# Performance work log

Hardware: AMD Instinct MI355X
Metric: run time of the kernel (lower is better)

Reference implementation:

```python
import jax, jax.numpy as jnp
import numpy as np

B, T = 256, 511          # batch, seq_len (512 - 1)
V = 128                  # tune_vocab_size
RV, MV, KV = 30, 20, 40  # rhythm/meter/key vocab sizes
E, ET = 16, 32           # context emb dim, tune emb dim
D = 3 * E + ET           # 80, LSTM input dim
H = 256                  # LSTM hidden


def setup_inputs() -> dict:
    key = jax.random.key(0)
    ks = jax.random.split(key, 14)
    s = 0.05
    return {
        "tune": jax.random.randint(ks[0], (B, T), 0, V + 1, dtype=jnp.int32),
        "rhythm": jax.random.randint(ks[1], (B, 1), 0, RV + 1, dtype=jnp.int32),
        "meter": jax.random.randint(ks[2], (B, 1), 0, MV + 1, dtype=jnp.int32),
        "key": jax.random.randint(ks[3], (B, 1), 0, KV + 1, dtype=jnp.int32),
        "tune_length": jax.random.randint(ks[4], (B, 1), 1, T, dtype=jnp.int32),
        # learned parameters
        "emb_rhythm": jax.random.normal(ks[5], (RV + 1, E), jnp.float32) * s,
        "emb_meter": jax.random.normal(ks[6], (MV + 1, E), jnp.float32) * s,
        "emb_key": jax.random.normal(ks[7], (KV + 1, E), jnp.float32) * s,
        "emb_tune": jax.random.normal(ks[8], (V + 1, ET), jnp.float32) * s,
        "W": jax.random.normal(ks[9], (D, 4 * H), jnp.float32) * s,   # input kernel (gates i,f,c,o)
        "U": jax.random.normal(ks[10], (H, 4 * H), jnp.float32) * s,  # recurrent kernel
        "b": jax.random.normal(ks[11], (4 * H,), jnp.float32) * s,
        "Wd": jax.random.normal(ks[12], (H, V), jnp.float32) * s,     # output dense
        "bd": jax.random.normal(ks[13], (V,), jnp.float32) * s,
    }


def reference(tune, rhythm, meter, key, tune_length,
              emb_rhythm, emb_meter, emb_key, emb_tune, W, U, b, Wd, bd):
    Bc, Tc = tune.shape
    Hc = U.shape[0]
    # conditioning context, repeated over time: [B, 48]
    ctx = jnp.concatenate(
        [emb_rhythm[rhythm[:, 0]], emb_meter[meter[:, 0]], emb_key[key[:, 0]]], axis=-1)
    # full LSTM input: [B, T, 80]
    x = jnp.concatenate(
        [jnp.broadcast_to(ctx[:, None, :], (Bc, Tc, ctx.shape[-1])), emb_tune[tune]], axis=-1)
    # sequence mask: step t valid iff t < tune_length  -> [B, T]
    mask = jnp.arange(Tc, dtype=tune_length.dtype)[None, :] < tune_length

    xs = jnp.swapaxes(x, 0, 1)   # [T, B, 80]
    ms = mask.T                  # [T, B]

    def step(carry, inp):
        h, c = carry
        xt, mt = inp
        z = xt @ W + h @ U + b                      # [B, 4H]
        i, f, g, o = jnp.split(z, 4, axis=-1)       # keras gate order i,f,c,o
        i = jax.nn.sigmoid(i)
        f = jax.nn.sigmoid(f)
        g = jnp.tanh(g)
        o = jax.nn.sigmoid(o)
        c_new = f * c + i * g
        h_new = o * jnp.tanh(c_new)
        m = mt[:, None]
        # masked steps: carry state through unchanged, output zeros
        h2 = jnp.where(m, h_new, h)
        c2 = jnp.where(m, c_new, c)
        out = jnp.where(m, h_new, jnp.zeros_like(h_new))
        return (h2, c2), out

    init = (jnp.zeros((Bc, Hc), x.dtype), jnp.zeros((Bc, Hc), x.dtype))
    _, ys = jax.lax.scan(step, init, (xs, ms))  # ys: [T, B, H]
    ys = jnp.swapaxes(ys, 0, 1)                 # [B, T, H]
    return ys @ Wd + bd                         # logits [B, T, V]
```

## Files before the change

### kernel.cpp

```cpp
#include <hip/hip_runtime.h>
#include <hip/hip_fp16.h>
#include <stdint.h>

#define BB 256
#define TT 511
#define VV 128
#define HH 256
#define G4 1024

typedef _Float16 h2_t __attribute__((ext_vector_type(2)));

__device__ __forceinline__ float fdot2(uint32_t a, uint32_t b, float c) {
  return __builtin_amdgcn_fdot2(__builtin_bit_cast(h2_t, a),
                                __builtin_bit_cast(h2_t, b), c, false);
}

__device__ __forceinline__ uint32_t pack2(float a, float b) {
  __half ha = __float2half(a), hb = __float2half(b);
  return (uint32_t)__half_as_ushort(ha) | ((uint32_t)__half_as_ushort(hb) << 16);
}


__global__ __launch_bounds__(1024) void prep_ctx_k(
    const int* __restrict__ rhythm, const int* __restrict__ meter, const int* __restrict__ keyi,
    const float* __restrict__ er, const float* __restrict__ em, const float* __restrict__ ek,
    const float* __restrict__ W, const float* __restrict__ bias, float* __restrict__ ctxW) {
  int b = blockIdx.x, j = threadIdx.x;
  int r = rhythm[b], m = meter[b], k = keyi[b];
  float acc = bias[j];
#pragma unroll
  for (int e = 0; e < 16; e++) acc += er[r*16+e] * W[(0+e)*G4 + j];
#pragma unroll
  for (int e = 0; e < 16; e++) acc += em[m*16+e] * W[(16+e)*G4 + j];
#pragma unroll
  for (int e = 0; e < 16; e++) acc += ek[k*16+e] * W[(32+e)*G4 + j];
  ctxW[b*G4 + j] = acc;
}

__global__ __launch_bounds__(1024) void prep_tune_k(
    const float* __restrict__ et, const float* __restrict__ W, float* __restrict__ tuneW) {
  int v = blockIdx.x, j = threadIdx.x;
  float acc = 0.f;
#pragma unroll
  for (int e = 0; e < 32; e++) acc += et[v*32+e] * W[(48+e)*G4 + j];
  tuneW[v*G4 + j] = acc;
}

__global__ __launch_bounds__(1024) void prep_U_k(
    const float* __restrict__ U, uint32_t* __restrict__ Up) {
  int kk = blockIdx.x, j = threadIdx.x;
  Up[kk*G4 + j] = pack2(U[(2*kk)*G4 + j], U[(2*kk+1)*G4 + j]);
}

__global__ __launch_bounds__(128) void prep_Wd_k(
    const float* __restrict__ Wd, uint32_t* __restrict__ Wdp) {
  int kp = blockIdx.x, v = threadIdx.x;
  Wdp[kp*VV + v] = pack2(Wd[(2*kp)*VV + v], Wd[(2*kp+1)*VV + v]);
}


#define NT 512
#define KREG 96
#define KLDS 32
#define RS 36
#define SMEM_BYTES (1024*RS*4 + 4096 + 512 + 2048)

__global__ __launch_bounds__(NT) void lstm_rec_k(
    const int* __restrict__ tune, const int* __restrict__ tlen,
    const uint32_t* __restrict__ Up, const float* __restrict__ ctxW,
    const float* __restrict__ tuneW, __half* __restrict__ h_hist) {
  extern __shared__ uint32_t smem[];
  uint32_t* Ulds = smem;
  float*    zbuf = (float*)(smem + 1024*RS);
  uint32_t* hpk  = (uint32_t*)(smem + 1024*RS + 1024);
  int*      tlds = (int*)(smem + 1024*RS + 1024 + 128);

  int b   = blockIdx.x;
  int tid = threadIdx.x;
  int L   = tlen[b];

  for (int i = tid; i < TT; i += NT) tlds[i] = tune[b*TT + i];
  if (tid < 128) hpk[tid] = 0u;

  uint32_t u0[KREG], u1[KREG];
#pragma unroll
  for (int kk = 0; kk < KREG; kk++) {
    u0[kk] = Up[kk*G4 + tid];
    u1[kk] = Up[kk*G4 + tid + NT];
  }
  for (int idx = tid; idx < KLDS*G4; idx += NT) {
    int kk = idx >> 10, j = idx & 1023;
    Ulds[j*RS + kk] = Up[(KREG+kk)*G4 + j];
  }
  float zc0 = ctxW[b*G4 + tid];
  float zc1 = ctxW[b*G4 + tid + NT];
  float cc  = 0.f;
  __syncthreads();

  const uint32_t* ur0 = Ulds + (size_t)tid*RS;
  const uint32_t* ur1 = Ulds + (size_t)(tid+NT)*RS;
  __half* hh_base = h_hist + (size_t)b*TT*HH;

  for (int t = 0; t < L; t++) {
    int v = tlds[t];
    float tw0 = tuneW[v*G4 + tid];
    float tw1 = tuneW[v*G4 + tid + NT];
    float a0 = 0.f, a1 = 0.f, d0 = 0.f, d1 = 0.f;
#pragma unroll
    for (int g = 0; g < KREG/4; g++) {
      uint4 h4 = *(const uint4*)(hpk + g*4);
      a0 = fdot2(h4.x, u0[4*g+0], a0);  a1 = fdot2(h4.x, u1[4*g+0], a1);
      d0 = fdot2(h4.y, u0[4*g+1], d0);  d1 = fdot2(h4.y, u1[4*g+1], d1);
      a0 = fdot2(h4.z, u0[4*g+2], a0);  a1 = fdot2(h4.z, u1[4*g+2], a1);
      d0 = fdot2(h4.w, u0[4*g+3], d0);  d1 = fdot2(h4.w, u1[4*g+3], d1);
    }
#pragma unroll
    for (int g = 0; g < KLDS/4; g++) {
      uint4 h4 = *(const uint4*)(hpk + KREG + g*4);
      uint4 ua = *(const uint4*)(ur0 + g*4);
      uint4 ub = *(const uint4*)(ur1 + g*4);
      a0 = fdot2(h4.x, ua.x, a0);  a1 = fdot2(h4.x, ub.x, a1);
      d0 = fdot2(h4.y, ua.y, d0);  d1 = fdot2(h4.y, ub.y, d1);
      a0 = fdot2(h4.z, ua.z, a0);  a1 = fdot2(h4.z, ub.z, a1);
      d0 = fdot2(h4.w, ua.w, d0);  d1 = fdot2(h4.w, ub.w, d1);
    }
    zbuf[tid]      = zc0 + tw0 + a0 + d0;
    zbuf[tid + NT] = zc1 + tw1 + a1 + d1;
    __syncthreads();
    if (tid < HH) {
      float zi = zbuf[tid];
      float zf = zbuf[tid + 256];
      float zg = zbuf[tid + 512];
      float zo = zbuf[tid + 768];
      float gi = 1.f / (1.f + __expf(-zi));
      float gf = 1.f / (1.f + __expf(-zf));
      float e2 = __expf(2.f*zg);
      float gg = (e2 - 1.f) / (e2 + 1.f);
      float go = 1.f / (1.f + __expf(-zo));
      cc = gf*cc + gi*gg;
      float ec = __expf(2.f*cc);
      float th = (ec - 1.f) / (ec + 1.f);
      float hv = go * th;
      __half hhv = __float2half(hv);
      ((__half*)hpk)[tid] = hhv;
      hh_base[(size_t)t*HH + tid] = hhv;
    }
    __syncthreads();
  }
}


__global__ __launch_bounds__(256) void out_gemm_k(
    const uint32_t* __restrict__ hsrc, const uint32_t* __restrict__ Wdp,
    const float* __restrict__ bd, const int* __restrict__ tlen,
    float* __restrict__ out) {
  __shared__ uint32_t A[64][128];
  int bb = blockIdx.x;
  int b  = bb >> 3, t0 = (bb & 7) << 6;
  int tid = threadIdx.x;
  int L = tlen[b];
  for (int idx = tid; idx < 64*128; idx += 256) {
    int r = idx >> 7, kp = idx & 127;
    int t = t0 + r;
    A[r][kp] = (t < TT) ? hsrc[((size_t)b*TT + t)*128 + kp] : 0u;
  }
  __syncthreads();
  int v = tid & 127, rg = tid >> 7;
  float acc[32];
#pragma unroll
  for (int r = 0; r < 32; r++) acc[r] = 0.f;
  for (int kb = 0; kb < 4; kb++) {
    uint32_t w[32];
#pragma unroll
    for (int q = 0; q < 32; q++) w[q] = Wdp[(kb*32+q)*VV + v];
#pragma unroll
    for (int r = 0; r < 32; r++) {
      const uint32_t* ar = &A[rg*32 + r][kb*32];
#pragma unroll
      for (int q4 = 0; q4 < 8; q4++) {
        uint4 a4 = *(const uint4*)(ar + q4*4);
        acc[r] = fdot2(a4.x, w[4*q4+0], acc[r]);
        acc[r] = fdot2(a4.y, w[4*q4+1], acc[r]);
        acc[r] = fdot2(a4.z, w[4*q4+2], acc[r]);
        acc[r] = fdot2(a4.w, w[4*q4+3], acc[r]);
      }
    }
  }
  float bias = bd[v];
#pragma unroll
  for (int r = 0; r < 32; r++) {
    int t = t0 + rg*32 + r;
    if (t < TT) {
      out[((size_t)b*TT + t)*VV + v] = (t < L) ? (acc[r] + bias) : bias;
    }
  }
}


extern "C" void kernel_launch(void* const* d_in, const int* in_sizes, int n_in,
                              void* d_out, int out_size, void* d_ws, size_t ws_size,
                              hipStream_t stream) {
  const int*   tune   = (const int*)d_in[0];
  const int*   rhythm = (const int*)d_in[1];
  const int*   meter  = (const int*)d_in[2];
  const int*   keyi   = (const int*)d_in[3];
  const int*   tlen   = (const int*)d_in[4];
  const float* er     = (const float*)d_in[5];
  const float* em     = (const float*)d_in[6];
  const float* ek     = (const float*)d_in[7];
  const float* et     = (const float*)d_in[8];
  const float* W      = (const float*)d_in[9];
  const float* U      = (const float*)d_in[10];
  const float* bias   = (const float*)d_in[11];
  const float* Wd     = (const float*)d_in[12];
  const float* bd     = (const float*)d_in[13];
  (void)in_sizes; (void)n_in; (void)out_size; (void)ws_size;

  char* ws = (char*)d_ws;
  uint32_t* Up    = (uint32_t*)(ws);
  float*    ctxW  = (float*)(ws + (512<<10));
  float*    tuneW = (float*)(ws + (512<<10) + (1024<<10));
  uint32_t* Wdp   = (uint32_t*)(ws + (512<<10) + (1024<<10) + (516<<10));

  hipFuncSetAttribute((const void*)lstm_rec_k,
                      hipFuncAttributeMaxDynamicSharedMemorySize, SMEM_BYTES);

  prep_ctx_k <<<BB,    1024, 0, stream>>>(rhythm, meter, keyi, er, em, ek, W, bias, ctxW);
  prep_tune_k<<<VV+1,  1024, 0, stream>>>(et, W, tuneW);
  prep_U_k   <<<128,   1024, 0, stream>>>(U, Up);
  prep_Wd_k  <<<128,   VV,   0, stream>>>(Wd, Wdp);
  lstm_rec_k <<<BB, NT, SMEM_BYTES, stream>>>(tune, tlen, Up, ctxW, tuneW, (__half*)d_out);
  out_gemm_k <<<BB*8,  256,  0, stream>>>((const uint32_t*)d_out, Wdp, bd, tlen, (float*)d_out);
}
```

Measured before the change: 951.6 us.

## Split recurrent matvec over K halves with readlane-broadcast hidden state

Restructures the LSTM recurrent matvec so each 256-thread half handles half of the hidden dimension and each thread computes four adjacent gate columns using uint4 register-resident weights. Hidden-state values are broadcast via readlane instead of repeated LDS vector loads, and partial sums from both halves are combined in the gate phase together with context terms now staged in LDS. This aims to reduce per-step LDS bandwidth, but raises register pressure and adds a cross-half reduction.

```diff
diff --git a/kernel.cpp b/kernel.cpp
--- a/kernel.cpp
+++ b/kernel.cpp
@@ -60,78 +60,88 @@
 
 
 #define NT 512
-#define KREG 96
-#define KLDS 32
-#define RS 36
-#define SMEM_BYTES (1024*RS*4 + 4096 + 512 + 2048)
+#define KREG 54
+#define KLDS 10
+#define ULDS_ROWS (2*KLDS)
+#define OFF_ZPART (ULDS_ROWS*G4)
+#define OFF_CTX   (OFF_ZPART + 2*G4)
+#define OFF_HBUF  (OFF_CTX + G4)
+#define OFF_TLDS  (OFF_HBUF + 128)
+#define SMEM_U32  (OFF_TLDS + 512)
+#define SMEM_BYTES (SMEM_U32*4)
 
 __global__ __launch_bounds__(NT) void lstm_rec_k(
     const int* __restrict__ tune, const int* __restrict__ tlen,
     const uint32_t* __restrict__ Up, const float* __restrict__ ctxW,
     const float* __restrict__ tuneW, __half* __restrict__ h_hist) {
   extern __shared__ uint32_t smem[];
-  uint32_t* Ulds = smem;
-  float*    zbuf = (float*)(smem + 1024*RS);
-  uint32_t* hpk  = (uint32_t*)(smem + 1024*RS + 1024);
-  int*      tlds = (int*)(smem + 1024*RS + 1024 + 128);
-
-  int b   = blockIdx.x;
-  int tid = threadIdx.x;
-  int L   = tlen[b];
+  uint32_t* Ulds   = smem;
+  float*    zpart  = (float*)(smem + OFF_ZPART);
+  float*    ctxlds = (float*)(smem + OFF_CTX);
+  uint32_t* hbuf   = smem + OFF_HBUF;
+  int*      tlds   = (int*)(smem + OFF_TLDS);
+
+  int b    = blockIdx.x;
+  int tid  = threadIdx.x;
+  int g    = tid >> 8;
+  int q    = tid & 255;
+  int lane = tid & 63;
+  int L    = tlen[b];
 
   for (int i = tid; i < TT; i += NT) tlds[i] = tune[b*TT + i];
-  if (tid < 128) hpk[tid] = 0u;
-
-  uint32_t u0[KREG], u1[KREG];
-#pragma unroll
-  for (int kk = 0; kk < KREG; kk++) {
-    u0[kk] = Up[kk*G4 + tid];
-    u1[kk] = Up[kk*G4 + tid + NT];
-  }
-  for (int idx = tid; idx < KLDS*G4; idx += NT) {
-    int kk = idx >> 10, j = idx & 1023;
-    Ulds[j*RS + kk] = Up[(KREG+kk)*G4 + j];
-  }
-  float zc0 = ctxW[b*G4 + tid];
-  float zc1 = ctxW[b*G4 + tid + NT];
-  float cc  = 0.f;
+  for (int i = tid; i < G4; i += NT) ctxlds[i] = ctxW[b*G4 + i];
+  if (tid < 128) hbuf[tid] = 0u;
+  for (int idx = tid; idx < ULDS_ROWS*G4; idx += NT) {
+    int row = idx >> 10, j = idx & 1023;
+    int gg = row / KLDS, r = row % KLDS;
+    Ulds[idx] = Up[(gg*64 + KREG + r)*G4 + j];
+  }
+
+  uint4 ureg[KREG];
+  {
+    const uint32_t* ubase = Up + (size_t)(g*64)*G4 + 4*q;
+#pragma unroll
+    for (int kk = 0; kk < KREG; kk++) ureg[kk] = *(const uint4*)(ubase + (size_t)kk*G4);
+  }
+  float cc = 0.f;
   __syncthreads();
 
-  const uint32_t* ur0 = Ulds + (size_t)tid*RS;
-  const uint32_t* ur1 = Ulds + (size_t)(tid+NT)*RS;
+  const uint32_t* uldsrow = Ulds + (size_t)(g*KLDS)*G4 + 4*q;
   __half* hh_base = h_hist + (size_t)b*TT*HH;
 
   for (int t = 0; t < L; t++) {
+    uint32_t vh = hbuf[g*64 + lane];
     int v = tlds[t];
-    float tw0 = tuneW[v*G4 + tid];
-    float tw1 = tuneW[v*G4 + tid + NT];
-    float a0 = 0.f, a1 = 0.f, d0 = 0.f, d1 = 0.f;
-#pragma unroll
-    for (int g = 0; g < KREG/4; g++) {
-      uint4 h4 = *(const uint4*)(hpk + g*4);
-      a0 = fdot2(h4.x, u0[4*g+0], a0);  a1 = fdot2(h4.x, u1[4*g+0], a1);
-      d0 = fdot2(h4.y, u0[4*g+1], d0);  d1 = fdot2(h4.y, u1[4*g+1], d1);
-      a0 = fdot2(h4.z, u0[4*g+2], a0);  a1 = fdot2(h4.z, u1[4*g+2], a1);
-      d0 = fdot2(h4.w, u0[4*g+3], d0);  d1 = fdot2(h4.w, u1[4*g+3], d1);
-    }
-#pragma unroll
-    for (int g = 0; g < KLDS/4; g++) {
-      uint4 h4 = *(const uint4*)(hpk + KREG + g*4);
-      uint4 ua = *(const uint4*)(ur0 + g*4);
-      uint4 ub = *(const uint4*)(ur1 + g*4);
-      a0 = fdot2(h4.x, ua.x, a0);  a1 = fdot2(h4.x, ub.x, a1);
-      d0 = fdot2(h4.y, ua.y, d0);  d1 = fdot2(h4.y, ub.y, d1);
-      a0 = fdot2(h4.z, ua.z, a0);  a1 = fdot2(h4.z, ub.z, a1);
-      d0 = fdot2(h4.w, ua.w, d0);  d1 = fdot2(h4.w, ub.w, d1);
-    }
-    zbuf[tid]      = zc0 + tw0 + a0 + d0;
-    zbuf[tid + NT] = zc1 + tw1 + a1 + d1;
+    float tw0, tw1, tw2, tw3;
+    if (tid < HH) {
+      const float* twp = tuneW + (size_t)v*G4 + tid;
+      tw0 = twp[0]; tw1 = twp[256]; tw2 = twp[512]; tw3 = twp[768];
+    }
+    float a0 = 0.f, a1 = 0.f, a2 = 0.f, a3 = 0.f;
+#pragma unroll
+    for (int kk = 0; kk < KREG; kk++) {
+      uint32_t hs = (uint32_t)__builtin_amdgcn_readlane((int)vh, kk);
+      a0 = fdot2(hs, ureg[kk].x, a0);
+      a1 = fdot2(hs, ureg[kk].y, a1);
+      a2 = fdot2(hs, ureg[kk].z, a2);
+      a3 = fdot2(hs, ureg[kk].w, a3);
+    }
+#pragma unroll
+    for (int r = 0; r < KLDS; r++) {
+      uint4 ul = *(const uint4*)(uldsrow + (size_t)r*G4);
+      uint32_t hs = (uint32_t)__builtin_amdgcn_readlane((int)vh, KREG + r);
+      a0 = fdot2(hs, ul.x, a0);
+      a1 = fdot2(hs, ul.y, a1);
+      a2 = fdot2(hs, ul.z, a2);
+      a3 = fdot2(hs, ul.w, a3);
+    }
+    *(float4*)(zpart + g*G4 + 4*q) = make_float4(a0, a1, a2, a3);
     __syncthreads();
     if (tid < HH) {
-      float zi = zbuf[tid];
-      float zf = zbuf[tid + 256];
-      float zg = zbuf[tid + 512];
-      float zo = zbuf[tid + 768];
+      float zi = zpart[tid      ] + zpart[G4 + tid      ] + ctxlds[tid      ] + tw0;
+      float zf = zpart[tid + 256] + zpart[G4 + tid + 256] + ctxlds[tid + 256] + tw1;
+      float zg = zpart[tid + 512] + zpart[G4 + tid + 512] + ctxlds[tid + 512] + tw2;
+      float zo = zpart[tid + 768] + zpart[G4 + tid + 768] + ctxlds[tid + 768] + tw3;
       float gi = 1.f / (1.f + __expf(-zi));
       float gf = 1.f / (1.f + __expf(-zf));
       float e2 = __expf(2.f*zg);
@@ -142,7 +152,7 @@
       float th = (ec - 1.f) / (ec + 1.f);
       float hv = go * th;
       __half hhv = __float2half(hv);
-      ((__half*)hpk)[tid] = hhv;
+      ((__half*)hbuf)[tid] = hhv;
       hh_base[(size_t)t*HH + tid] = hhv;
     }
     __syncthreads();
```

After: 1.029 ms. 1.08x slower.
